# Kernel optimization log

Measured on AMD Instinct MI355X. Metric: run time of the kernel, lower is better.

The kernel has to match this reference:

```python
import jax, jax.numpy as jnp
import numpy as np

S, B, H = 2048, 2, 2048
NP = 16            # num attention heads
HN = H // NP       # head dim = 128


def setup_inputs() -> dict:
    key = jax.random.key(0)
    k0, k1, k2 = jax.random.split(key, 3)
    hidden_states = jax.random.normal(k0, (S, B, H), dtype=jnp.float32) * 0.02
    w_qkv = jax.random.normal(k1, (3 * H, H), dtype=jnp.float32) * 0.02
    b_qkv = jnp.zeros((3 * H,), dtype=jnp.float32)
    w_dense = jax.random.normal(k2, (H, H), dtype=jnp.float32) * 0.02
    b_dense = jnp.zeros((H,), dtype=jnp.float32)
    # causal mask: True means "mask out" (strictly upper triangular)
    attention_mask = jnp.triu(jnp.ones((S, S), dtype=bool), k=1)[None, None]  # [1,1,S,S]
    return {
        "hidden_states": hidden_states,
        "attention_mask": attention_mask,
        "w_qkv": w_qkv,
        "b_qkv": b_qkv,
        "w_dense": w_dense,
        "b_dense": b_dense,
    }


def reference(hidden_states, attention_mask, w_qkv, b_qkv, w_dense, b_dense):
    s, b, h = hidden_states.shape
    # fused QKV projection (ColumnParallelLinear: y = x @ W^T + b)
    mixed = hidden_states @ w_qkv.T + b_qkv                 # [s,b,3h]
    mixed = mixed.reshape(s, b, NP, 3 * HN)
    q, k, v = jnp.split(mixed, 3, axis=-1)                  # each [s,b,np,hn]
    norm = 1.0 / jnp.sqrt(jnp.asarray(HN, hidden_states.dtype))
    # scaled QK^T -> [b,np,sq,sk]
    scores = jnp.einsum("sbnh,tbnh->bnst", q, k) * norm
    # attention_mask_func: masked_fill(mask, -10000.0)
    scores = jnp.where(attention_mask, jnp.asarray(-10000.0, scores.dtype), scores)
    # softmax in fp32 (softmax_in_fp32)
    probs = jax.nn.softmax(scores.astype(jnp.float32), axis=-1).astype(scores.dtype)
    # AV matmul -> [s,b,np,hn] -> [s,b,h]
    context = jnp.einsum("bnst,tbnh->sbnh", probs, v).reshape(s, b, h)
    # output projection (RowParallelLinear)
    out = context @ w_dense.T + b_dense
    return out
```

## Files before the change

kernel.cpp:

```cpp
#include <hip/hip_runtime.h>
#include <hip/hip_bf16.h>
#include <cstdint>
#include <cstddef>

#define SS   2048
#define BB   2
#define HH   2048
#define NHEAD 16
#define HDIM 128
#define H3   6144
#define MROWS 4096

typedef __attribute__((ext_vector_type(4))) float f32x4;
typedef __attribute__((ext_vector_type(8))) __bf16 bf16x8;
typedef __attribute__((ext_vector_type(8))) unsigned short us8;
typedef __attribute__((ext_vector_type(4))) unsigned short us4;

__device__ __forceinline__ unsigned short f2b(float f) {
    union { float f; unsigned u; } v; v.f = f;
    unsigned r = v.u + 0x7fffu + ((v.u >> 16) & 1u);
    return (unsigned short)(r >> 16);
}

__device__ __forceinline__ bf16x8 ld_b16x8(const unsigned short* p) {
    us8 u = *(const us8*)p;
    return __builtin_bit_cast(bf16x8, u);
}

__device__ __forceinline__ bf16x8 ld8_off(const unsigned short* base, int byteoff) {
    return __builtin_bit_cast(bf16x8, *(const us8*)((const char*)base + byteoff));
}

__device__ __forceinline__ int sw256(int b) { return b ^ (((b >> 8) & 7) << 4); }
__device__ __forceinline__ int sw128(int b) { return b ^ (((b >> 7) & 7) << 4); }

__device__ __forceinline__ void gload_lds16(const unsigned short* g, unsigned short* l) {
    __builtin_amdgcn_global_load_lds(
        (const __attribute__((address_space(1))) unsigned int*)g,
        (__attribute__((address_space(3))) unsigned int*)l, 16, 0, 0);
}

__global__ __launch_bounds__(256) void cvt_f32_bf16(
    const float* __restrict__ in, unsigned short* __restrict__ out, int n4)
{
    const int stride = gridDim.x * blockDim.x;
    for (int i = blockIdx.x * blockDim.x + threadIdx.x; i < n4; i += stride) {
        const float4 v = ((const float4*)in)[i];
        us4 o = { f2b(v.x), f2b(v.y), f2b(v.z), f2b(v.w) };
        ((us4*)out)[i] = o;
    }
}

__global__ __launch_bounds__(256) void transpose_v(
    const unsigned short* __restrict__ mixed,
    unsigned short* __restrict__ vt)
{
    const int st = blockIdx.x;
    const int nh = blockIdx.y;
    const int bb = blockIdx.z;
    const int tid = threadIdx.x;
    __shared__ unsigned short T[64][136];
#pragma unroll
    for (int i = 0; i < 4; ++i) {
        const int c = i * 256 + tid;
        const int sl = c >> 4, d0 = (c & 15) << 3;
        const us8 v = *(const us8*)(mixed +
            ((size_t)(st * 64 + sl) * BB + bb) * H3 + nh * 384 + 256 + d0);
        *(us8*)(&T[sl][d0]) = v;
    }
    __syncthreads();
#pragma unroll
    for (int i = 0; i < 4; ++i) {
        const int c = i * 256 + tid;
        const int d = c >> 3, sl0 = (c & 7) << 3;
        us8 o;
#pragma unroll
        for (int j = 0; j < 8; ++j) o[j] = T[sl0 + j][d];
        *(us8*)(vt + ((size_t)(bb * NHEAD + nh) * HDIM + d) * SS + st * 64 + sl0) = o;
    }
}

#define STAGE_UNIT(gp, lo)                                        \
    gload_lds16((gp) + soff[0], smem + (lo) + tid * 8);           \
    gload_lds16((gp) + soff[1], smem + (lo) + 4096 + tid * 8);

template <int BN, bool F32OUT>
__global__ __launch_bounds__(512, 2) void gemm_8ph(
    const unsigned short* __restrict__ A,
    const unsigned short* __restrict__ Bw,
    const float* __restrict__ bias,
    void* __restrict__ Cout,
    int Nv, int Kv)
{
    extern __shared__ unsigned short smem[];
    constexpr int NF     = BN / 64;
    constexpr int BUNITS = BN / 128;
    constexpr int BELEMS = BN * 64;

    const int tid  = threadIdx.x;
    const int lane = tid & 63;
    const int wave = tid >> 6;
    const int wm = wave >> 2, wn = wave & 3;
    const int bm = blockIdx.y, bn = blockIdx.x;

    const unsigned short* Ab = A  + (size_t)bm * 128 * Kv;
    const unsigned short* Bb = Bw + (size_t)bn * BN * Kv;

    int soff[2];
#pragma unroll
    for (int i = 0; i < 2; ++i) {
        const int p = (i * 512 + tid) * 16;
        const int l = p ^ (((p >> 7) & 7) << 4);
        soff[i] = (l >> 7) * Kv + ((l & 127) >> 1);
    }

    f32x4 acc[4][NF];
#pragma unroll
    for (int m = 0; m < 4; ++m)
#pragma unroll
        for (int n = 0; n < NF; ++n) acc[m][n] = (f32x4){0.f, 0.f, 0.f, 0.f};

    const int frow = lane & 15;
    const int g16  = (lane >> 4) << 4;
    const int swx  = (frow & 7) << 4;
    const int kx0  = g16 ^ swx;
    const int kx1  = (64 + g16) ^ swx;
    const int aRow = (wm * 64 + frow) * 128;
    const int bRow = 32768 + (wn * (BN / 4) + frow) * 128;

    const int NT = Kv >> 6;

    STAGE_UNIT(Ab, 0);
    STAGE_UNIT(Bb, 16384);
    STAGE_UNIT(Bb + 128 * Kv, 16384 + 8192);
    if constexpr (BUNITS == 3) { STAGE_UNIT(Bb + 256 * Kv, 16384 + 16384); }
    STAGE_UNIT(Bb + 64, 16384 + BELEMS);
    STAGE_UNIT(Bb + 128 * Kv + 64, 16384 + BELEMS + 8192);
    if constexpr (BUNITS == 3) { STAGE_UNIT(Bb + 256 * Kv + 64, 16384 + BELEMS + 16384); }
    if constexpr (BUNITS == 3) { asm volatile("s_waitcnt vmcnt(6)" ::: "memory"); }
    else                       { asm volatile("s_waitcnt vmcnt(4)" ::: "memory"); }
    __builtin_amdgcn_s_barrier();

    for (int t = 0; t < NT; ++t) {
        const int j  = t & 1;
        const int jn = j ^ 1;
        const int aj = j * 16384;
        const int bj = j * (BN * 128);
        const int cA = ((t + 1 < NT) ? (t + 1) : (NT - 1)) * 64;
        const int cB = ((t + 2 < NT) ? (t + 2) : (NT - 1)) * 64;

        bf16x8 bbf[NF][2];

        {
            bf16x8 a0 = ld8_off(smem, aj + aRow + 0 * 2048 + kx0);
            bf16x8 a1 = ld8_off(smem, aj + aRow + 0 * 2048 + kx1);
#pragma unroll
            for (int n = 0; n < NF; ++n) {
                bbf[n][0] = ld8_off(smem, bj + bRow + n * 2048 + kx0);
                bbf[n][1] = ld8_off(smem, bj + bRow + n * 2048 + kx1);
            }
            STAGE_UNIT(Ab + cA, jn * 8192);
            __builtin_amdgcn_s_barrier();
            asm volatile("s_waitcnt lgkmcnt(0)" ::: "memory");
            __builtin_amdgcn_sched_barrier(0);
            __builtin_amdgcn_s_setprio(1);
#pragma unroll
            for (int n = 0; n < NF; ++n) {
                acc[0][n] = __builtin_amdgcn_mfma_f32_16x16x32_bf16(a0, bbf[n][0], acc[0][n], 0, 0, 0);
                acc[0][n] = __builtin_amdgcn_mfma_f32_16x16x32_bf16(a1, bbf[n][1], acc[0][n], 0, 0, 0);
            }
            __builtin_amdgcn_s_setprio(0);
            __builtin_amdgcn_s_barrier();
        }
        {
            bf16x8 a0 = ld8_off(smem, aj + aRow + 1 * 2048 + kx0);
            bf16x8 a1 = ld8_off(smem, aj + aRow + 1 * 2048 + kx1);
            STAGE_UNIT(Bb + cB, 16384 + j * BELEMS);
            __builtin_amdgcn_s_barrier();
            asm volatile("s_waitcnt lgkmcnt(0)" ::: "memory");
            __builtin_amdgcn_sched_barrier(0);
            __builtin_amdgcn_s_setprio(1);
#pragma unroll
            for (int n = 0; n < NF; ++n) {
                acc[1][n] = __builtin_amdgcn_mfma_f32_16x16x32_bf16(a0, bbf[n][0], acc[1][n], 0, 0, 0);
                acc[1][n] = __builtin_amdgcn_mfma_f32_16x16x32_bf16(a1, bbf[n][1], acc[1][n], 0, 0, 0);
            }
            __builtin_amdgcn_s_setprio(0);
            __builtin_amdgcn_s_barrier();
        }
        {
            bf16x8 a0 = ld8_off(smem, aj + aRow + 2 * 2048 + kx0);
            bf16x8 a1 = ld8_off(smem, aj + aRow + 2 * 2048 + kx1);
            STAGE_UNIT(Bb + 128 * Kv + cB, 16384 + j * BELEMS + 8192);
            __builtin_amdgcn_s_barrier();
            asm volatile("s_waitcnt lgkmcnt(0)" ::: "memory");
            __builtin_amdgcn_sched_barrier(0);
            __builtin_amdgcn_s_setprio(1);
#pragma unroll
            for (int n = 0; n < NF; ++n) {
                acc[2][n] = __builtin_amdgcn_mfma_f32_16x16x32_bf16(a0, bbf[n][0], acc[2][n], 0, 0, 0);
                acc[2][n] = __builtin_amdgcn_mfma_f32_16x16x32_bf16(a1, bbf[n][1], acc[2][n], 0, 0, 0);
            }
            __builtin_amdgcn_s_setprio(0);
            __builtin_amdgcn_s_barrier();
        }
        {
            bf16x8 a0 = ld8_off(smem, aj + aRow + 3 * 2048 + kx0);
            bf16x8 a1 = ld8_off(smem, aj + aRow + 3 * 2048 + kx1);
            if constexpr (BUNITS == 3) {
                STAGE_UNIT(Bb + 256 * Kv + cB, 16384 + j * BELEMS + 16384);
            }
            __builtin_amdgcn_s_barrier();
            asm volatile("s_waitcnt lgkmcnt(0)" ::: "memory");
            __builtin_amdgcn_sched_barrier(0);
            __builtin_amdgcn_s_setprio(1);
#pragma unroll
            for (int n = 0; n < NF; ++n) {
                acc[3][n] = __builtin_amdgcn_mfma_f32_16x16x32_bf16(a0, bbf[n][0], acc[3][n], 0, 0, 0);
                acc[3][n] = __builtin_amdgcn_mfma_f32_16x16x32_bf16(a1, bbf[n][1], acc[3][n], 0, 0, 0);
            }
            __builtin_amdgcn_s_setprio(0);
            if constexpr (BUNITS == 3) { asm volatile("s_waitcnt vmcnt(6)" ::: "memory"); }
            else                       { asm volatile("s_waitcnt vmcnt(4)" ::: "memory"); }
            __builtin_amdgcn_s_barrier();
        }
    }

    const int r0 = (lane >> 4) << 2;
#pragma unroll
    for (int m = 0; m < 4; ++m) {
        const int row = bm * 128 + wm * 64 + m * 16 + r0;
#pragma unroll
        for (int n = 0; n < NF; ++n) {
            const int col = bn * BN + wn * (BN / 4) + n * 16 + frow;
            const float bv = bias[col];
#pragma unroll
            for (int r = 0; r < 4; ++r) {
                const float o = acc[m][n][r] + bv;
                if (F32OUT) ((float*)Cout)[(size_t)(row + r) * Nv + col] = o;
                else        ((unsigned short*)Cout)[(size_t)(row + r) * Nv + col] = f2b(o);
            }
        }
    }
}

template <bool F32OUT>
__global__ __launch_bounds__(256) void gemm_lds(
    const unsigned short* __restrict__ A,
    const unsigned short* __restrict__ Bw,
    const float* __restrict__ bias,
    void* __restrict__ Cout,
    int Nv, int Kv)
{
    __shared__ unsigned short Ash[128 * 64];
    __shared__ unsigned short Bsh[128 * 64];

    const int tid  = threadIdx.x;
    const int lane = tid & 63;
    const int wave = tid >> 6;
    const int wm = wave >> 1, wn = wave & 1;
    const int bm = blockIdx.y, bn = blockIdx.x;

    const unsigned short* Ab = A  + (size_t)bm * 128 * Kv;
    const unsigned short* Bb = Bw + (size_t)bn * 128 * Kv;

    int srcoff[4];
#pragma unroll
    for (int i = 0; i < 4; ++i) {
        const int p0 = (i * 256 + tid) * 16;
        const int l0 = p0 ^ (((p0 >> 7) & 7) << 4);
        srcoff[i] = (l0 >> 7) * Kv + ((l0 & 127) >> 1);
    }

    f32x4 acc[4][4];
#pragma unroll
    for (int m = 0; m < 4; ++m)
#pragma unroll
        for (int n = 0; n < 4; ++n) acc[m][n] = (f32x4){0.f, 0.f, 0.f, 0.f};

    const int frow = lane & 15;
    const int g16  = (lane >> 4) << 4;
    const int swx  = (frow & 7) << 4;

    for (int kt = 0; kt < Kv; kt += 64) {
#pragma unroll
        for (int i = 0; i < 4; ++i) {
            gload_lds16(Ab + srcoff[i] + kt, Ash + (i * 2048 + wave * 512));
            gload_lds16(Bb + srcoff[i] + kt, Bsh + (i * 2048 + wave * 512));
        }
        __syncthreads();

#pragma unroll
        for (int ks = 0; ks < 2; ++ks) {
            bf16x8 af[4], bfr[4];
#pragma unroll
            for (int m = 0; m < 4; ++m)
                af[m] = ld8_off(Ash, (((wm * 64 + m * 16 + frow) << 7) + ks * 64 + g16) ^ swx);
#pragma unroll
            for (int n = 0; n < 4; ++n)
                bfr[n] = ld8_off(Bsh, (((wn * 64 + n * 16 + frow) << 7) + ks * 64 + g16) ^ swx);
#pragma unroll
            for (int m = 0; m < 4; ++m)
#pragma unroll
                for (int n = 0; n < 4; ++n)
                    acc[m][n] = __builtin_amdgcn_mfma_f32_16x16x32_bf16(af[m], bfr[n], acc[m][n], 0, 0, 0);
        }
        __syncthreads();
    }

    const int r0 = (lane >> 4) << 2;
#pragma unroll
    for (int m = 0; m < 4; ++m) {
        const int row = bm * 128 + wm * 64 + m * 16 + r0;
#pragma unroll
        for (int n = 0; n < 4; ++n) {
            const int col = bn * 128 + wn * 64 + n * 16 + frow;
            const float bv = bias[col];
#pragma unroll
            for (int r = 0; r < 4; ++r) {
                const float o = acc[m][n][r] + bv;
                if (F32OUT) ((float*)Cout)[(size_t)(row + r) * Nv + col] = o;
                else        ((unsigned short*)Cout)[(size_t)(row + r) * Nv + col] = f2b(o);
            }
        }
    }
}

__global__ __launch_bounds__(256) void attn_kernel(
    const unsigned short* __restrict__ mixed,
    const unsigned short* __restrict__ vt,
    unsigned short* __restrict__ context)
{
    const int pair = blockIdx.x;
    const int nh   = blockIdx.y;
    const int bb   = blockIdx.z;
    const int tid  = threadIdx.x;
    const int lane = tid & 63;
    const int wave = tid >> 6;

    __shared__ __align__(1024) unsigned short smem[16384 + 16384 + 4096];

    const int frow = lane & 15;
    const int g16  = (lane >> 4) << 4;
    const int r0   = (lane >> 4) << 2;

    int koff[4], voff[4];
#pragma unroll
    for (int i = 0; i < 4; ++i) {
        const int p0 = (i * 256 + tid) * 16;
        const int lK = p0 ^ (((p0 >> 8) & 7) << 4);
        koff[i] = (lK >> 8) * (BB * H3) + ((lK & 255) >> 1);
        const int lV = p0 ^ (((p0 >> 7) & 7) << 4);
        voff[i] = (lV >> 7) * SS + ((lV & 127) >> 1);
    }

    const unsigned short* kg = mixed + (size_t)bb * H3 + nh * 384 + 128;
    const unsigned short* vg = vt + (size_t)(bb * NHEAD + nh) * HDIM * SS;

    const float norm = 0.088388347648318447f;
    char* Pb = (char*)(smem + 32768) + wave * 2048;

    for (int half = 0; half < 2; ++half) {
        const int qt = half ? (31 - pair) : pair;
        const int q0 = qt * 64 + wave * 16;

        bf16x8 qf[4];
        {
            const unsigned short* qptr =
                mixed + ((size_t)(q0 + frow) * BB + bb) * H3 + nh * 384;
#pragma unroll
            for (int kk = 0; kk < 4; ++kk)
                qf[kk] = ld_b16x8(qptr + kk * 32 + ((lane >> 4) << 3));
        }

        f32x4 Oacc[8];
#pragma unroll
        for (int ct = 0; ct < 8; ++ct) Oacc[ct] = (f32x4){0.f, 0.f, 0.f, 0.f};
        float m_r[4] = {-1e30f, -1e30f, -1e30f, -1e30f};
        float l_r[4] = {0.f, 0.f, 0.f, 0.f};

        {
            unsigned short* Kd = smem + wave * 512;
            unsigned short* Vd = smem + 16384 + wave * 512;
#pragma unroll
            for (int i = 0; i < 4; ++i) {
                gload_lds16(kg + koff[i], Kd + i * 2048);
                gload_lds16(vg + voff[i], Vd + i * 2048);
            }
        }
        __syncthreads();

        int cur = 0;
        for (int kt = 0; kt <= qt; ++kt) {
            if (kt < qt) {
                const unsigned short* kt_g = kg + (size_t)(kt + 1) * 64 * (BB * H3);
                const unsigned short* vt_g = vg + (kt + 1) * 64;
                unsigned short* Kd = smem + (cur ^ 1) * 8192 + wave * 512;
                unsigned short* Vd = smem + 16384 + (cur ^ 1) * 8192 + wave * 512;
#pragma unroll
                for (int i = 0; i < 4; ++i) {
                    gload_lds16(kt_g + koff[i], Kd + i * 2048);
                    gload_lds16(vt_g + voff[i], Vd + i * 2048);
                }
            }

            const unsigned short* Ks = smem + cur * 8192;
            const unsigned short* Vs = smem + 16384 + cur * 8192;
            const int krow0 = kt * 64;

            f32x4 sc4[4];
#pragma unroll
            for (int t = 0; t < 4; ++t) {
                f32x4 s = (f32x4){0.f, 0.f, 0.f, 0.f};
#pragma unroll
                for (int kk = 0; kk < 4; ++kk) {
                    bf16x8 kf = ld8_off(Ks, sw256((t * 16 + frow) * 256 + kk * 64 + g16));
                    s = __builtin_amdgcn_mfma_f32_16x16x32_bf16(qf[kk], kf, s, 0, 0, 0);
                }
                sc4[t] = s;
            }

#pragma unroll
            for (int t = 0; t < 4; ++t) {
                const int kcol = krow0 + t * 16 + frow;
#pragma unroll
                for (int r = 0; r < 4; ++r) {
                    float sv = sc4[t][r] * norm;
                    if (kcol > q0 + r0 + r) sv = -1e30f;
                    sc4[t][r] = sv;
                }
            }

            float tmax[4];
#pragma unroll
            for (int r = 0; r < 4; ++r)
                tmax[r] = fmaxf(fmaxf(sc4[0][r], sc4[1][r]), fmaxf(sc4[2][r], sc4[3][r]));
#pragma unroll
            for (int r = 0; r < 4; ++r) {
                tmax[r] = fmaxf(tmax[r], __shfl_xor(tmax[r], 1, 64));
                tmax[r] = fmaxf(tmax[r], __shfl_xor(tmax[r], 2, 64));
                tmax[r] = fmaxf(tmax[r], __shfl_xor(tmax[r], 4, 64));
                tmax[r] = fmaxf(tmax[r], __shfl_xor(tmax[r], 8, 64));
            }

            float a_r[4], rsum[4];
#pragma unroll
            for (int r = 0; r < 4; ++r) {
                const float mnew = fmaxf(m_r[r], tmax[r]);
                a_r[r] = __expf(m_r[r] - mnew);
                m_r[r] = mnew;
                rsum[r] = 0.f;
            }
#pragma unroll
            for (int t = 0; t < 4; ++t)
#pragma unroll
                for (int r = 0; r < 4; ++r) {
                    const float p = __expf(sc4[t][r] - m_r[r]);
                    sc4[t][r] = p;
                    rsum[r] += p;
                }
#pragma unroll
            for (int r = 0; r < 4; ++r) {
                rsum[r] += __shfl_xor(rsum[r], 1, 64);
                rsum[r] += __shfl_xor(rsum[r], 2, 64);
                rsum[r] += __shfl_xor(rsum[r], 4, 64);
                rsum[r] += __shfl_xor(rsum[r], 8, 64);
                l_r[r] = l_r[r] * a_r[r] + rsum[r];
            }
#pragma unroll
            for (int ct = 0; ct < 8; ++ct)
#pragma unroll
                for (int r = 0; r < 4; ++r) Oacc[ct][r] *= a_r[r];

#pragma unroll
            for (int t = 0; t < 4; ++t)
#pragma unroll
                for (int r = 0; r < 4; ++r)
                    *(unsigned short*)(Pb + sw128((r0 + r) * 128 + (t * 16 + frow) * 2)) =
                        f2b(sc4[t][r]);

#pragma unroll
            for (int ks = 0; ks < 2; ++ks) {
                bf16x8 pf = ld8_off((const unsigned short*)Pb, sw128(frow * 128 + ks * 64 + g16));
#pragma unroll
                for (int ct = 0; ct < 8; ++ct) {
                    bf16x8 vf = ld8_off(Vs, sw128((ct * 16 + frow) * 128 + ks * 64 + g16));
                    Oacc[ct] = __builtin_amdgcn_mfma_f32_16x16x32_bf16(pf, vf, Oacc[ct], 0, 0, 0);
                }
            }

            __syncthreads();
            cur ^= 1;
        }

#pragma unroll
        for (int ct = 0; ct < 8; ++ct) {
            const int d = ct * 16 + frow;
#pragma unroll
            for (int r = 0; r < 4; ++r) {
                const float o = Oacc[ct][r] / l_r[r];
                const size_t row = (size_t)(q0 + r0 + r) * BB + bb;
                context[row * HH + nh * 128 + d] = f2b(o);
            }
        }
    }
}

extern "C" void kernel_launch(void* const* d_in, const int* in_sizes, int n_in,
                              void* d_out, int out_size, void* d_ws, size_t ws_size,
                              hipStream_t stream) {
    const float* hidden  = (const float*)d_in[0];
    const float* w_qkv   = (const float*)d_in[2];
    const float* b_qkv   = (const float*)d_in[3];
    const float* w_dense = (const float*)d_in[4];
    const float* b_dense = (const float*)d_in[5];
    float* out = (float*)d_out;

    unsigned short* mixed = (unsigned short*)d_ws;
    unsigned short* hb    = mixed + (size_t)MROWS * H3;
    unsigned short* wq    = hb + (size_t)MROWS * HH;
    unsigned short* wd    = wq + (size_t)H3 * HH;
    unsigned short* context = hb;
    unsigned short* vtg     = wq;

    dim3 blk(256);
    cvt_f32_bf16<<<2048, blk, 0, stream>>>(hidden, hb, (MROWS * HH) / 4);
    cvt_f32_bf16<<<2048, blk, 0, stream>>>(w_qkv, wq, (H3 * HH) / 4);
    cvt_f32_bf16<<<1024, blk, 0, stream>>>(w_dense, wd, (HH * HH) / 4);

    hipFuncSetAttribute(reinterpret_cast<const void*>(gemm_8ph<384, false>),
                        hipFuncAttributeMaxDynamicSharedMemorySize, 131072);
    gemm_8ph<384, false><<<dim3(H3 / 384, MROWS / 128), dim3(512), 131072, stream>>>(
        hb, wq, b_qkv, mixed, H3, HH);
    transpose_v<<<dim3(32, NHEAD, BB), blk, 0, stream>>>(mixed, vtg);
    attn_kernel<<<dim3(16, NHEAD, BB), blk, 0, stream>>>(mixed, vtg, context);
    gemm_lds<true><<<dim3(16, 32), blk, 0, stream>>>(context, wd, b_dense, out, HH, HH);
}
```

Measured before the change: 279.0 us.

## Use pipelined 8-phase GEMM for dense projection and drop trailing phase barriers

Replaces the simple LDS-staged gemm_lds used for the output projection with the 8-wave, multi-phase pipelined gemm_8ph template (BN=256, fp32 output). It also removes the barrier at the end of each of the four compute phases in the 8-phase loop, relying on the barrier before each phase's MFMAs. This targets the dense GEMM's unoverlapped load/compute and extra synchronization, but dropping the barriers risks LDS write-after-read races between stages.

Result: faster. 270.5 us (-3.1%).

```diff
diff --git a/kernel.cpp b/kernel.cpp
--- a/kernel.cpp
+++ b/kernel.cpp
@@ -170,7 +170,6 @@
                 acc[0][n] = __builtin_amdgcn_mfma_f32_16x16x32_bf16(a1, bbf[n][1], acc[0][n], 0, 0, 0);
             }
             __builtin_amdgcn_s_setprio(0);
-            __builtin_amdgcn_s_barrier();
         }
         {
             bf16x8 a0 = ld8_off(smem, aj + aRow + 1 * 2048 + kx0);
@@ -186,7 +185,6 @@
                 acc[1][n] = __builtin_amdgcn_mfma_f32_16x16x32_bf16(a1, bbf[n][1], acc[1][n], 0, 0, 0);
             }
             __builtin_amdgcn_s_setprio(0);
-            __builtin_amdgcn_s_barrier();
         }
         {
             bf16x8 a0 = ld8_off(smem, aj + aRow + 2 * 2048 + kx0);
@@ -202,7 +200,6 @@
                 acc[2][n] = __builtin_amdgcn_mfma_f32_16x16x32_bf16(a1, bbf[n][1], acc[2][n], 0, 0, 0);
             }
             __builtin_amdgcn_s_setprio(0);
-            __builtin_amdgcn_s_barrier();
         }
         {
             bf16x8 a0 = ld8_off(smem, aj + aRow + 3 * 2048 + kx0);
@@ -222,7 +219,6 @@
             __builtin_amdgcn_s_setprio(0);
             if constexpr (BUNITS == 3) { asm volatile("s_waitcnt vmcnt(6)" ::: "memory"); }
             else                       { asm volatile("s_waitcnt vmcnt(4)" ::: "memory"); }
-            __builtin_amdgcn_s_barrier();
         }
     }
 
@@ -233,88 +229,6 @@
 #pragma unroll
         for (int n = 0; n < NF; ++n) {
             const int col = bn * BN + wn * (BN / 4) + n * 16 + frow;
-            const float bv = bias[col];
-#pragma unroll
-            for (int r = 0; r < 4; ++r) {
-                const float o = acc[m][n][r] + bv;
-                if (F32OUT) ((float*)Cout)[(size_t)(row + r) * Nv + col] = o;
-                else        ((unsigned short*)Cout)[(size_t)(row + r) * Nv + col] = f2b(o);
-            }
-        }
-    }
-}
-
-template <bool F32OUT>
-__global__ __launch_bounds__(256) void gemm_lds(
-    const unsigned short* __restrict__ A,
-    const unsigned short* __restrict__ Bw,
-    const float* __restrict__ bias,
-    void* __restrict__ Cout,
-    int Nv, int Kv)
-{
-    __shared__ unsigned short Ash[128 * 64];
-    __shared__ unsigned short Bsh[128 * 64];
-
-    const int tid  = threadIdx.x;
-    const int lane = tid & 63;
-    const int wave = tid >> 6;
-    const int wm = wave >> 1, wn = wave & 1;
-    const int bm = blockIdx.y, bn = blockIdx.x;
-
-    const unsigned short* Ab = A  + (size_t)bm * 128 * Kv;
-    const unsigned short* Bb = Bw + (size_t)bn * 128 * Kv;
-
-    int srcoff[4];
-#pragma unroll
-    for (int i = 0; i < 4; ++i) {
-        const int p0 = (i * 256 + tid) * 16;
-        const int l0 = p0 ^ (((p0 >> 7) & 7) << 4);
-        srcoff[i] = (l0 >> 7) * Kv + ((l0 & 127) >> 1);
-    }
-
-    f32x4 acc[4][4];
-#pragma unroll
-    for (int m = 0; m < 4; ++m)
-#pragma unroll
-        for (int n = 0; n < 4; ++n) acc[m][n] = (f32x4){0.f, 0.f, 0.f, 0.f};
-
-    const int frow = lane & 15;
-    const int g16  = (lane >> 4) << 4;
-    const int swx  = (frow & 7) << 4;
-
-    for (int kt = 0; kt < Kv; kt += 64) {
-#pragma unroll
-        for (int i = 0; i < 4; ++i) {
-            gload_lds16(Ab + srcoff[i] + kt, Ash + (i * 2048 + wave * 512));
-            gload_lds16(Bb + srcoff[i] + kt, Bsh + (i * 2048 + wave * 512));
-        }
-        __syncthreads();
-
-#pragma unroll
-        for (int ks = 0; ks < 2; ++ks) {
-            bf16x8 af[4], bfr[4];
-#pragma unroll
-            for (int m = 0; m < 4; ++m)
-                af[m] = ld8_off(Ash, (((wm * 64 + m * 16 + frow) << 7) + ks * 64 + g16) ^ swx);
-#pragma unroll
-            for (int n = 0; n < 4; ++n)
-                bfr[n] = ld8_off(Bsh, (((wn * 64 + n * 16 + frow) << 7) + ks * 64 + g16) ^ swx);
-#pragma unroll
-            for (int m = 0; m < 4; ++m)
-#pragma unroll
-                for (int n = 0; n < 4; ++n)
-                    acc[m][n] = __builtin_amdgcn_mfma_f32_16x16x32_bf16(af[m], bfr[n], acc[m][n], 0, 0, 0);
-        }
-        __syncthreads();
-    }
-
-    const int r0 = (lane >> 4) << 2;
-#pragma unroll
-    for (int m = 0; m < 4; ++m) {
-        const int row = bm * 128 + wm * 64 + m * 16 + r0;
-#pragma unroll
-        for (int n = 0; n < 4; ++n) {
-            const int col = bn * 128 + wn * 64 + n * 16 + frow;
             const float bv = bias[col];
 #pragma unroll
             for (int r = 0; r < 4; ++r) {
@@ -534,5 +448,8 @@
         hb, wq, b_qkv, mixed, H3, HH);
     transpose_v<<<dim3(32, NHEAD, BB), blk, 0, stream>>>(mixed, vtg);
     attn_kernel<<<dim3(16, NHEAD, BB), blk, 0, stream>>>(mixed, vtg, context);
-    gemm_lds<true><<<dim3(16, 32), blk, 0, stream>>>(context, wd, b_dense, out, HH, HH);
-}
+    hipFuncSetAttribute(reinterpret_cast<const void*>(gemm_8ph<256, true>),
+                        hipFuncAttributeMaxDynamicSharedMemorySize, 98304);
+    gemm_8ph<256, true><<<dim3(HH / 256, MROWS / 128), dim3(512), 98304, stream>>>(
+        context, wd, b_dense, out, HH, HH);
+}
```
